# Optimization experiments

Measured on AMD Instinct MI355X. Metric: run time of the kernel, lower is better.

The kernel has to match this reference:

```python
import jax, jax.numpy as jnp
import numpy as np
from jax import lax

DN = ('NCHW', 'OIHW', 'NCHW')

def conv3x3(x, w):
    return lax.conv_general_dilated(x, w, (1, 1), 'SAME', dimension_numbers=DN)

def conv1x1(x, w, b):
    # w: [O, C], x: [B, C, H, W]
    return jnp.einsum('oc,bchw->bohw', w, x) + b[None, :, None, None]

def bn_relu(x, p):
    # p: [2, C] -> (scale, shift), eval-mode folded BatchNorm + ReLU
    return jax.nn.relu(x * p[0][None, :, None, None] + p[1][None, :, None, None])

def pam(y, Wb, bb, Wc, bc, Wd, bd, alpha):
    B, C, H, W = y.shape
    n = H * W
    b_ = conv1x1(y, Wb, bb).reshape(B, -1, n)   # [B, C/8, N]
    c_ = conv1x1(y, Wc, bc).reshape(B, -1, n)   # [B, C/8, N]
    d_ = conv1x1(y, Wd, bd).reshape(B, C, n)    # [B, C, N]
    energy = jnp.einsum('bkn,bkm->bnm', b_, c_)  # [B, N, N]
    attn = jax.nn.softmax(energy, axis=-1)
    feat = jnp.einsum('bcm,bnm->bcn', d_, attn).reshape(B, C, H, W)
    return alpha[0] * feat + y

def cam(y, beta):
    B, C, H, W = y.shape
    xf = y.reshape(B, C, H * W)
    energy = jnp.einsum('bcn,bdn->bcd', xf, xf)  # [B, C, C]
    energy = jnp.max(energy, axis=-1, keepdims=True) - energy
    attn = jax.nn.softmax(energy, axis=-1)
    feat = jnp.einsum('bcd,bdn->bcn', attn, xf).reshape(B, C, H, W)
    return beta[0] * feat + y

def reference(x, Wp1, bnp1, Wc1, bnc1, Wb, bb, Wc, bc, Wd, bd, alpha, beta,
              Wp2, bnp2, Wc2, bnc2, Wout, bout, Wp3, bp3, Wc3, bc3):
    feat_p = bn_relu(conv3x3(x, Wp1), bnp1)
    feat_p = pam(feat_p, Wb, bb, Wc, bc, Wd, bd, alpha)
    feat_p = bn_relu(conv3x3(feat_p, Wp2), bnp2)

    feat_c = bn_relu(conv3x3(x, Wc1), bnc1)
    feat_c = cam(feat_c, beta)
    feat_c = bn_relu(conv3x3(feat_c, Wc2), bnc2)

    fusion = feat_p + feat_c
    out_main = jax.nn.sigmoid(conv1x1(fusion, Wout, bout))
    out_p = jax.nn.sigmoid(conv1x1(feat_p, Wp3, bp3))
    out_c = jax.nn.sigmoid(conv1x1(feat_c, Wc3, bc3))
    return (out_main, out_p, out_c)

def setup_inputs() -> dict:
    key = jax.random.key(0)
    ks = jax.random.split(key, 24)
    Cin, Ci, Ck, NC = 512, 128, 16, 19
    B, H, W = 8, 64, 64
    s = lambda k, shape, scale=0.05: jax.random.normal(k, shape, jnp.float32) * scale
    return {
        'x': jax.random.normal(ks[0], (B, Cin, H, W), jnp.float32),
        'Wp1': s(ks[1], (Ci, Cin, 3, 3)), 'bnp1': jnp.stack([jnp.ones(Ci), jnp.zeros(Ci)]),
        'Wc1': s(ks[2], (Ci, Cin, 3, 3)), 'bnc1': jnp.stack([jnp.ones(Ci), jnp.zeros(Ci)]),
        'Wb': s(ks[3], (Ck, Ci)), 'bb': s(ks[4], (Ck,)),
        'Wc': s(ks[5], (Ck, Ci)), 'bc': s(ks[6], (Ck,)),
        'Wd': s(ks[7], (Ci, Ci)), 'bd': s(ks[8], (Ci,)),
        'alpha': jax.random.normal(ks[9], (1,), jnp.float32) * 0.5,
        'beta': jax.random.normal(ks[10], (1,), jnp.float32) * 0.5,
        'Wp2': s(ks[11], (Ci, Ci, 3, 3)), 'bnp2': jnp.stack([jnp.ones(Ci), jnp.zeros(Ci)]),
        'Wc2': s(ks[12], (Ci, Ci, 3, 3)), 'bnc2': jnp.stack([jnp.ones(Ci), jnp.zeros(Ci)]),
        'Wout': s(ks[13], (NC, Ci)), 'bout': s(ks[14], (NC,)),
        'Wp3': s(ks[15], (NC, Ci)), 'bp3': s(ks[16], (NC,)),
        'Wc3': s(ks[17], (NC, Ci)), 'bc3': s(ks[18], (NC,)),
    }
```

## Files before the change

kernel.cpp:

```cpp
#include <hip/hip_runtime.h>
#include <math.h>


typedef __attribute__((ext_vector_type(8)))  short short8;
typedef __attribute__((ext_vector_type(16))) float f32x16;

__device__ inline unsigned short f2bf(float f) {
    union { float f; unsigned u; } v; v.f = f;
    unsigned r = v.u + 0x7fffu + ((v.u >> 16) & 1u);
    return (unsigned short)(r >> 16);
}
__device__ inline float bf2f(unsigned short h) {
    union { unsigned u; float f; } v; v.u = ((unsigned)h) << 16;
    return v.f;
}

__global__ __launch_bounds__(256) void wpack_kernel(
    const float* __restrict__ W, unsigned short* __restrict__ wp, int Cin, int total)
{
    int idx = blockIdx.x * 256 + threadIdx.x;
    if (idx >= total) return;
    int chunk = idx / 18432;
    int rem   = idx - chunk * 18432;
    int tap   = rem >> 11;
    int rem2  = rem & 2047;
    int co    = rem2 >> 4;
    int ci    = rem2 & 15;
    int cin   = (chunk << 4) + ci;
    wp[idx] = f2bf(W[((size_t)co * Cin + cin) * 9 + tap]);
}

__global__ __launch_bounds__(256) void wpack_split_kernel(
    const float* __restrict__ W, unsigned short* __restrict__ wph,
    unsigned short* __restrict__ wpl, int Cin, int total)
{
    int idx = blockIdx.x * 256 + threadIdx.x;
    if (idx >= total) return;
    int chunk = idx / 18432;
    int rem   = idx - chunk * 18432;
    int tap   = rem >> 11;
    int rem2  = rem & 2047;
    int co    = rem2 >> 4;
    int ci    = rem2 & 15;
    int cin   = (chunk << 4) + ci;
    float w = W[((size_t)co * Cin + cin) * 9 + tap];
    unsigned short hi = f2bf(w);
    wph[idx] = hi;
    wpl[idx] = f2bf(w - bf2f(hi));
}

__global__ __launch_bounds__(256) void conv3x3_mfma(
    const void* __restrict__ xin, int in_is_fp32, int Cin,
    const unsigned short* __restrict__ wpack, const float* __restrict__ bn,
    float* __restrict__ out_f32, unsigned short* __restrict__ out_bf)
{
    const int t   = threadIdx.x;
    const int w   = t >> 6;
    const int wy  = w >> 1;
    const int wx  = w & 1;
    const int ln  = t & 63;
    const int l31 = ln & 31;
    const int g   = ln >> 5;
    const int y0  = blockIdx.x << 1;
    const int co0 = blockIdx.y << 6;
    const int b   = blockIdx.z;

    __shared__ __align__(16) unsigned short Xl[4 * 66 * 16];
    __shared__ __align__(16) unsigned short Wl[9 * 64 * 16];

    const f32x16 zero = {0,0,0,0,0,0,0,0,0,0,0,0,0,0,0,0};
    f32x16 acc0 = zero, acc1 = zero;

    const int nchunks = Cin >> 4;
    for (int ch = 0; ch < nchunks; ++ch) {
        const int cin0 = ch << 4;
        for (int pid = t; pid < 264; pid += 256) {
            int r  = pid / 66;
            int xc = pid - r * 66;
            int gy = y0 - 1 + r;
            int gx = xc - 1;
            unsigned short tmp[16];
            if ((unsigned)gy < 64u && (unsigned)gx < 64u) {
                if (in_is_fp32) {
                    const float* src = (const float*)xin
                        + (((size_t)b * Cin + cin0) << 12) + (gy << 6) + gx;
#pragma unroll
                    for (int c = 0; c < 16; c++) tmp[c] = f2bf(src[(size_t)c << 12]);
                } else {
                    const unsigned short* src = (const unsigned short*)xin
                        + (((size_t)b * Cin + cin0) << 12) + (gy << 6) + gx;
#pragma unroll
                    for (int c = 0; c < 16; c++) tmp[c] = src[(size_t)c << 12];
                }
            } else {
#pragma unroll
                for (int c = 0; c < 16; c++) tmp[c] = 0;
            }
            *(uint4*)&Xl[pid * 16 + 0] = ((uint4*)tmp)[0];
            *(uint4*)&Xl[pid * 16 + 8] = ((uint4*)tmp)[1];
        }
        {
            const uint4* wsrc = (const uint4*)wpack;
            const int base = ch * 2304 + (co0 << 1);
            for (int idx = t; idx < 1152; idx += 256)
                ((uint4*)Wl)[idx] = wsrc[base + ((idx >> 7) << 8) + (idx & 127)];
        }
        __syncthreads();

#pragma unroll 3
        for (int tap = 0; tap < 9; ++tap) {
            const int dy = tap / 3, dx = tap - dy * 3;
            short8 a = *(const short8*)&Wl[((tap << 6) + (wy << 5) + l31) * 16 + (g << 3)];
            const int row = wx + dy;
            short8 b0 = *(const short8*)&Xl[(row * 66 + l31 + dx) * 16 + (g << 3)];
            short8 b1 = *(const short8*)&Xl[(row * 66 + l31 + 32 + dx) * 16 + (g << 3)];
            acc0 = __builtin_amdgcn_mfma_f32_32x32x16_bf16(a, b0, acc0, 0, 0, 0);
            acc1 = __builtin_amdgcn_mfma_f32_32x32x16_bf16(a, b1, acc1, 0, 0, 0);
        }
        __syncthreads();
    }

    const int y = y0 + wx;
#pragma unroll
    for (int j = 0; j < 2; j++) {
        const f32x16 a = j ? acc1 : acc0;
#pragma unroll
        for (int r = 0; r < 16; r++) {
            int co = co0 + (wy << 5) + (r & 3) + ((r >> 2) << 3) + (g << 2);
            int x  = (j << 5) + l31;
            float v = fmaf(a[r], bn[co], bn[128 + co]);
            v = v > 0.f ? v : 0.f;
            size_t o = (((size_t)b * 128 + co) << 12) + (y << 6) + x;
            if (out_f32) out_f32[o] = v;
            if (out_bf)  out_bf[o]  = f2bf(v);
        }
    }
}

__global__ __launch_bounds__(256) void conv3x3_mfma_hilo(
    const float* __restrict__ xin, int Cin,
    const unsigned short* __restrict__ wph, const unsigned short* __restrict__ wpl,
    const float* __restrict__ bn, float* __restrict__ out_f32,
    unsigned short* __restrict__ outh, unsigned short* __restrict__ outl)
{
    const int t   = threadIdx.x;
    const int w   = t >> 6;
    const int wy  = w >> 1;
    const int wx  = w & 1;
    const int ln  = t & 63;
    const int l31 = ln & 31;
    const int g   = ln >> 5;
    const int y0  = blockIdx.x << 1;
    const int co0 = blockIdx.y << 6;
    const int b   = blockIdx.z;

    __shared__ __align__(16) unsigned short Xh[4 * 66 * 16];
    __shared__ __align__(16) unsigned short Xo[4 * 66 * 16];
    __shared__ __align__(16) unsigned short Wh[9 * 64 * 16];
    __shared__ __align__(16) unsigned short Wo[9 * 64 * 16];

    const f32x16 zero = {0,0,0,0,0,0,0,0,0,0,0,0,0,0,0,0};
    f32x16 acc0 = zero, acc1 = zero;

    const int nchunks = Cin >> 4;
    for (int ch = 0; ch < nchunks; ++ch) {
        const int cin0 = ch << 4;
        for (int pid = t; pid < 264; pid += 256) {
            int r  = pid / 66;
            int xc = pid - r * 66;
            int gy = y0 - 1 + r;
            int gx = xc - 1;
            unsigned short th[16], tl[16];
            if ((unsigned)gy < 64u && (unsigned)gx < 64u) {
                const float* src = xin + (((size_t)b * Cin + cin0) << 12) + (gy << 6) + gx;
#pragma unroll
                for (int c = 0; c < 16; c++) {
                    float f = src[(size_t)c << 12];
                    unsigned short hi = f2bf(f);
                    th[c] = hi;
                    tl[c] = f2bf(f - bf2f(hi));
                }
            } else {
#pragma unroll
                for (int c = 0; c < 16; c++) { th[c] = 0; tl[c] = 0; }
            }
            *(uint4*)&Xh[pid * 16 + 0] = ((uint4*)th)[0];
            *(uint4*)&Xh[pid * 16 + 8] = ((uint4*)th)[1];
            *(uint4*)&Xo[pid * 16 + 0] = ((uint4*)tl)[0];
            *(uint4*)&Xo[pid * 16 + 8] = ((uint4*)tl)[1];
        }
        {
            const uint4* sh = (const uint4*)wph;
            const uint4* sl = (const uint4*)wpl;
            const int base = ch * 2304 + (co0 << 1);
            for (int idx = t; idx < 1152; idx += 256) {
                int o = base + ((idx >> 7) << 8) + (idx & 127);
                ((uint4*)Wh)[idx] = sh[o];
                ((uint4*)Wo)[idx] = sl[o];
            }
        }
        __syncthreads();

#pragma unroll 1
        for (int tap = 0; tap < 9; ++tap) {
            const int dy = tap / 3, dx = tap - dy * 3;
            const int wi = ((tap << 6) + (wy << 5) + l31) * 16 + (g << 3);
            const int row = wx + dy;
            const int xi0 = (row * 66 + l31 + dx) * 16 + (g << 3);
            const int xi1 = (row * 66 + l31 + 32 + dx) * 16 + (g << 3);
            short8 ah = *(const short8*)&Wh[wi];
            short8 al = *(const short8*)&Wo[wi];
            short8 b0h = *(const short8*)&Xh[xi0];
            short8 b1h = *(const short8*)&Xh[xi1];
            short8 b0l = *(const short8*)&Xo[xi0];
            short8 b1l = *(const short8*)&Xo[xi1];
            acc0 = __builtin_amdgcn_mfma_f32_32x32x16_bf16(ah, b0h, acc0, 0, 0, 0);
            acc1 = __builtin_amdgcn_mfma_f32_32x32x16_bf16(ah, b1h, acc1, 0, 0, 0);
            acc0 = __builtin_amdgcn_mfma_f32_32x32x16_bf16(ah, b0l, acc0, 0, 0, 0);
            acc1 = __builtin_amdgcn_mfma_f32_32x32x16_bf16(ah, b1l, acc1, 0, 0, 0);
            acc0 = __builtin_amdgcn_mfma_f32_32x32x16_bf16(al, b0h, acc0, 0, 0, 0);
            acc1 = __builtin_amdgcn_mfma_f32_32x32x16_bf16(al, b1h, acc1, 0, 0, 0);
        }
        __syncthreads();
    }

    const int y = y0 + wx;
#pragma unroll
    for (int j = 0; j < 2; j++) {
        const f32x16 a = j ? acc1 : acc0;
#pragma unroll
        for (int r = 0; r < 16; r++) {
            int co = co0 + (wy << 5) + (r & 3) + ((r >> 2) << 3) + (g << 2);
            int x  = (j << 5) + l31;
            float v = fmaf(a[r], bn[co], bn[128 + co]);
            v = v > 0.f ? v : 0.f;
            size_t o = (((size_t)b * 128 + co) << 12) + (y << 6) + x;
            out_f32[o] = v;
            if (outh) {
                unsigned short hi = f2bf(v);
                outh[o] = hi;
                outl[o] = f2bf(v - bf2f(hi));
            }
        }
    }
}

__global__ __launch_bounds__(256) void cam_energy_mfma(
    const unsigned short* __restrict__ bh, const unsigned short* __restrict__ bl,
    float* __restrict__ egy_part)
{
    const int t   = threadIdx.x;
    const int w   = t >> 6;
    const int ln  = t & 63;
    const int l31 = ln & 31;
    const int g   = ln >> 5;
    const int i0  = (blockIdx.x >> 2) << 5;
    const int j0  = (blockIdx.x & 3) << 5;
    const int nseg = blockIdx.y;
    const int b   = blockIdx.z;

    __shared__ float red[4][64][17];

    const f32x16 zero = {0,0,0,0,0,0,0,0,0,0,0,0,0,0,0,0};
    f32x16 acc = zero;
    const int nb = (nseg << 9) + (w << 7) + (g << 3);
    const size_t ri = ((size_t)b * 128 + i0 + l31) << 12;
    const size_t rj = ((size_t)b * 128 + j0 + l31) << 12;

#pragma unroll
    for (int c = 0; c < 8; c++) {
        const int n0 = nb + (c << 4);
        short8 ah  = *(const short8*)(bh + ri + n0);
        short8 al  = *(const short8*)(bl + ri + n0);
        short8 bhf = *(const short8*)(bh + rj + n0);
        short8 blf = *(const short8*)(bl + rj + n0);
        acc = __builtin_amdgcn_mfma_f32_32x32x16_bf16(ah, bhf, acc, 0, 0, 0);
        acc = __builtin_amdgcn_mfma_f32_32x32x16_bf16(ah, blf, acc, 0, 0, 0);
        acc = __builtin_amdgcn_mfma_f32_32x32x16_bf16(al, bhf, acc, 0, 0, 0);
    }
#pragma unroll
    for (int r = 0; r < 16; r++) red[w][ln][r] = acc[r];
    __syncthreads();

    const int lane = t & 63;
    const int rq   = t >> 6;
    float* base = egy_part + (((size_t)(nseg * 8 + b)) << 14);
#pragma unroll
    for (int e = 0; e < 4; e++) {
        const int reg = (rq << 2) + e;
        float v = red[0][lane][reg] + red[1][lane][reg]
                + red[2][lane][reg] + red[3][lane][reg];
        const int i = i0 + (reg & 3) + ((reg >> 2) << 3) + ((lane >> 5) << 2);
        base[i * 128 + j0 + (lane & 31)] = v;
    }
}

__global__ __launch_bounds__(256) void cam_softmax_fused(
    const float* __restrict__ egy_part, float* __restrict__ egy)
{
    const int b   = blockIdx.x;
    const int rg  = blockIdx.y;
    const int t   = threadIdx.x;
    const int row = (rg << 4) + (t >> 4);
    const int jg  = t & 15;

    float e[8];
#pragma unroll
    for (int jj = 0; jj < 8; jj++) e[jj] = 0.f;
    for (int seg = 0; seg < 8; seg++) {
        const float* p = egy_part + (((size_t)(seg * 8 + b)) << 14) + row * 128 + (jg << 3);
#pragma unroll
        for (int jj = 0; jj < 8; jj++) e[jj] += p[jj];
    }
    float mn = e[0];
#pragma unroll
    for (int jj = 1; jj < 8; jj++) mn = fminf(mn, e[jj]);
#pragma unroll
    for (int k = 1; k < 16; k <<= 1) mn = fminf(mn, __shfl_xor(mn, k));
    float s = 0.f;
#pragma unroll
    for (int jj = 0; jj < 8; jj++) { float p = __expf(mn - e[jj]); e[jj] = p; s += p; }
#pragma unroll
    for (int k = 1; k < 16; k <<= 1) s += __shfl_xor(s, k);
    const float inv = 1.f / s;
    float* orow = egy + ((size_t)b << 14) + row * 128 + (jg << 3);
#pragma unroll
    for (int jj = 0; jj < 8; jj++) orow[jj] = e[jj] * inv;
}

__global__ __launch_bounds__(256) void pam_qk_1x1(
    const float* __restrict__ A, const float* __restrict__ Wb, const float* __restrict__ bb,
    const float* __restrict__ Wc, const float* __restrict__ bc,
    unsigned short* __restrict__ qt, unsigned short* __restrict__ kt)
{
    __shared__ float wl[2 * 16 * 128];
    __shared__ float bl[32];
    const int t = threadIdx.x;
    const int n = (blockIdx.x << 8) + t;
    const int b = blockIdx.y;
    for (int idx = t; idx < 2048; idx += 256) { wl[idx] = Wb[idx]; wl[2048 + idx] = Wc[idx]; }
    if (t < 16) { bl[t] = bb[t]; bl[16 + t] = bc[t]; }
    __syncthreads();
    float ab[16], ac[16];
#pragma unroll
    for (int k = 0; k < 16; k++) { ab[k] = 0.f; ac[k] = 0.f; }
    for (int chn = 0; chn < 128; ++chn) {
        float a = A[(((size_t)b * 128 + chn) << 12) + n];
#pragma unroll
        for (int k = 0; k < 16; k++) {
            ab[k] = fmaf(wl[k * 128 + chn], a, ab[k]);
            ac[k] = fmaf(wl[2048 + k * 128 + chn], a, ac[k]);
        }
    }
    unsigned short uq[16], uk[16];
#pragma unroll
    for (int k = 0; k < 16; k++) {
        uq[k] = f2bf(ab[k] + bl[k]);
        uk[k] = f2bf(ac[k] + bl[16 + k]);
    }
    size_t row = (size_t)b * 4096 + n;
    ((uint4*)qt)[row * 2 + 0] = ((uint4*)uq)[0];
    ((uint4*)qt)[row * 2 + 1] = ((uint4*)uq)[1];
    ((uint4*)kt)[row * 2 + 0] = ((uint4*)uk)[0];
    ((uint4*)kt)[row * 2 + 1] = ((uint4*)uk)[1];
}

__global__ __launch_bounds__(256) void pam_v_1x1(
    const float* __restrict__ A, const float* __restrict__ Wd, const float* __restrict__ bd,
    unsigned short* __restrict__ vb)
{
    __shared__ float wl[32 * 128];
    __shared__ float bl[32];
    const int t   = threadIdx.x;
    const int n   = (blockIdx.x << 8) + t;
    const int co0 = blockIdx.y << 5;
    const int b   = blockIdx.z;
    for (int idx = t; idx < 4096; idx += 256) {
        int c2 = idx >> 7, chv = idx & 127;
        wl[idx] = Wd[(co0 + c2) * 128 + chv];
    }
    if (t < 32) bl[t] = bd[co0 + t];
    __syncthreads();
    float acc[32];
#pragma unroll
    for (int k = 0; k < 32; k++) acc[k] = 0.f;
    for (int chn = 0; chn < 128; ++chn) {
        float a = A[(((size_t)b * 128 + chn) << 12) + n];
#pragma unroll
        for (int k = 0; k < 32; k++) acc[k] = fmaf(wl[k * 128 + chn], a, acc[k]);
    }
#pragma unroll
    for (int k = 0; k < 32; k++)
        vb[(((size_t)b * 128 + co0 + k) << 12) + n] = f2bf(acc[k] + bl[k]);
}

__global__ __launch_bounds__(256) void pam_rowmax(
    const unsigned short* __restrict__ qt, const unsigned short* __restrict__ kt,
    float* __restrict__ rowmax)
{
    const int t  = threadIdx.x;
    const int w  = t >> 6;
    const int L  = t & 63;
    const int ln = L & 31;
    const int g  = L >> 5;
    const int b  = blockIdx.y;
    const int n0 = blockIdx.x << 5;
    __shared__ float red[4][32];

    const f32x16 zero = {0,0,0,0,0,0,0,0,0,0,0,0,0,0,0,0};
    short8 qfrag = *(const short8*)(qt + (((size_t)b * 4096 + n0 + ln) << 4) + (g << 3));

    float mx = -INFINITY;
    for (int mq = (w << 5); mq < 4096; mq += 128) {
        short8 kfrag = *(const short8*)(kt + (((size_t)b * 4096 + mq + ln) << 4) + (g << 3));
        f32x16 s = __builtin_amdgcn_mfma_f32_32x32x16_bf16(kfrag, qfrag, zero, 0, 0, 0);
#pragma unroll
        for (int r = 0; r < 16; r++) mx = fmaxf(mx, s[r]);
    }
    mx = fmaxf(mx, __shfl_xor(mx, 32));
    if (L < 32) red[w][L] = mx;
    __syncthreads();
    if (t < 32) {
        float m = fmaxf(fmaxf(red[0][t], red[1][t]), fmaxf(red[2][t], red[3][t]));
        rowmax[((size_t)b << 12) + n0 + t] = m;
    }
}

__global__ __launch_bounds__(256) void pam_attn_mfma(
    const unsigned short* __restrict__ qt, const unsigned short* __restrict__ kt,
    const unsigned short* __restrict__ vb, const float* __restrict__ rowmax,
    const float* __restrict__ alpha, const float* __restrict__ Y,
    unsigned short* __restrict__ outb)
{
    const int t  = threadIdx.x;
    const int w  = t >> 6;
    const int L  = t & 63;
    const int ln = L & 31;
    const int g  = L >> 5;
    const int b  = blockIdx.y;
    const int n0 = blockIdx.x << 5;
    const int c0 = w << 5;

    __shared__ unsigned short Pf[16 * 256];
    __shared__ float red[4][32];

    const f32x16 zero = {0,0,0,0,0,0,0,0,0,0,0,0,0,0,0,0};
    short8 qfrag = *(const short8*)(qt + (((size_t)b * 4096 + n0 + ln) << 4) + (g << 3));
    const float rm = rowmax[((size_t)b << 12) + n0 + ln];
    const float al = alpha[0];

    f32x16 acc = zero;
    float rs = 0.f;

    for (int m0 = 0; m0 < 4096; m0 += 128) {
        const int mq = m0 + (w << 5);
        short8 kfrag = *(const short8*)(kt + (((size_t)b * 4096 + mq + ln) << 4) + (g << 3));
        f32x16 s = __builtin_amdgcn_mfma_f32_32x32x16_bf16(kfrag, qfrag, zero, 0, 0, 0);

        float p[16];
#pragma unroll
        for (int r = 0; r < 16; r++) { p[r] = __expf(s[r] - rm); rs += p[r]; }
        float xx[16];
#pragma unroll
        for (int r = 0; r < 16; r++) xx[r] = __shfl_xor(p[r], 32);

        unsigned short f0[8], f1[8];
#pragma unroll
        for (int i = 0; i < 4; i++) {
            f0[i]     = f2bf(g ? xx[4 + i]  : p[i]);
            f0[4 + i] = f2bf(g ? p[4 + i]   : xx[i]);
            f1[i]     = f2bf(g ? xx[12 + i] : p[8 + i]);
            f1[4 + i] = f2bf(g ? p[12 + i]  : xx[8 + i]);
        }
        *(short8*)(&Pf[((w << 2) + g) * 256 + (ln << 3)])     = *(short8*)f0;
        *(short8*)(&Pf[((w << 2) + 2 + g) * 256 + (ln << 3)]) = *(short8*)f1;
        __syncthreads();

#pragma unroll
        for (int kk = 0; kk < 8; kk++) {
            short8 pfrag = *(const short8*)(&Pf[((kk << 1) + g) * 256 + (ln << 3)]);
            short8 vfrag = *(const short8*)(vb + (((size_t)b * 128 + c0 + ln) << 12)
                                               + m0 + (kk << 4) + (g << 3));
            acc = __builtin_amdgcn_mfma_f32_32x32x16_bf16(vfrag, pfrag, acc, 0, 0, 0);
        }
        __syncthreads();
    }

    rs += __shfl_xor(rs, 32);
    if (L < 32) red[w][L] = rs;
    __syncthreads();
    const float inv = 1.f / (red[0][ln] + red[1][ln] + red[2][ln] + red[3][ln]);
    const int n = n0 + ln;
#pragma unroll
    for (int r = 0; r < 16; r++) {
        int c = c0 + (r & 3) + ((r >> 2) << 3) + (g << 2);
        size_t idx = (((size_t)b * 128 + c) << 12) + n;
        outb[idx] = f2bf(fmaf(al, acc[r] * inv, Y[idx]));
    }
}

__global__ __launch_bounds__(256) void cam_feat(
    const float* __restrict__ attn, const float* __restrict__ Bf,
    const float* __restrict__ beta, float* __restrict__ outf)
{
    const int t  = threadIdx.x;
    const int n  = (blockIdx.x << 8) + t;
    const int c0 = blockIdx.y << 5;
    const int b  = blockIdx.z;
    __shared__ float al[32 * 128];
    for (int idx = t; idx < 4096; idx += 256)
        al[idx] = attn[(size_t)b * 16384 + (c0 + (idx >> 7)) * 128 + (idx & 127)];
    __syncthreads();
    float acc[32];
#pragma unroll
    for (int k = 0; k < 32; k++) acc[k] = 0.f;
    for (int d = 0; d < 128; ++d) {
        float v = Bf[(((size_t)b * 128 + d) << 12) + n];
#pragma unroll
        for (int k = 0; k < 32; k++) acc[k] = fmaf(al[k * 128 + d], v, acc[k]);
    }
    float be = beta[0];
#pragma unroll
    for (int k = 0; k < 32; k++) {
        size_t idx = (((size_t)b * 128 + c0 + k) << 12) + n;
        outf[idx] = fmaf(be, acc[k], Bf[idx]);
    }
}

__global__ __launch_bounds__(256) void heads(
    const float* __restrict__ FP, const float* __restrict__ FC,
    const float* __restrict__ Wout, const float* __restrict__ bout,
    const float* __restrict__ Wp3, const float* __restrict__ bp3,
    const float* __restrict__ Wc3, const float* __restrict__ bc3,
    float* __restrict__ out)
{
    const int t = threadIdx.x;
    const int n = (blockIdx.x << 8) + t;
    const int b = blockIdx.y;
    __shared__ float wl[3 * 19 * 128];
    __shared__ float bl[3 * 19];
    for (int idx = t; idx < 2432; idx += 256) {
        wl[idx]        = Wout[idx];
        wl[2432 + idx] = Wp3[idx];
        wl[4864 + idx] = Wc3[idx];
    }
    if (t < 19) { bl[t] = bout[t]; bl[19 + t] = bp3[t]; bl[38 + t] = bc3[t]; }
    __syncthreads();
    float am[19], ap[19], ac[19];
#pragma unroll
    for (int o = 0; o < 19; o++) { am[o] = 0.f; ap[o] = 0.f; ac[o] = 0.f; }
    for (int chn = 0; chn < 128; ++chn) {
        float pv = FP[(((size_t)b * 128 + chn) << 12) + n];
        float cv = FC[(((size_t)b * 128 + chn) << 12) + n];
        float fv = pv + cv;
#pragma unroll
        for (int o = 0; o < 19; o++) {
            am[o] = fmaf(wl[o * 128 + chn], fv, am[o]);
            ap[o] = fmaf(wl[2432 + o * 128 + chn], pv, ap[o]);
            ac[o] = fmaf(wl[4864 + o * 128 + chn], cv, ac[o]);
        }
    }
    const size_t OS = (size_t)8 * 19 * 4096;
#pragma unroll
    for (int o = 0; o < 19; o++) {
        size_t base = (((size_t)b * 19 + o) << 12) + n;
        out[base]          = 1.f / (1.f + __expf(-(am[o] + bl[o])));
        out[OS + base]     = 1.f / (1.f + __expf(-(ap[o] + bl[19 + o])));
        out[2 * OS + base] = 1.f / (1.f + __expf(-(ac[o] + bl[38 + o])));
    }
}

extern "C" void kernel_launch(void* const* d_in, const int* in_sizes, int n_in,
                              void* d_out, int out_size, void* d_ws, size_t ws_size,
                              hipStream_t stream)
{
    const float* x     = (const float*)d_in[0];
    const float* Wp1   = (const float*)d_in[1];
    const float* bnp1  = (const float*)d_in[2];
    const float* Wc1   = (const float*)d_in[3];
    const float* bnc1  = (const float*)d_in[4];
    const float* Wb    = (const float*)d_in[5];
    const float* bb    = (const float*)d_in[6];
    const float* Wc    = (const float*)d_in[7];
    const float* bcv   = (const float*)d_in[8];
    const float* Wd    = (const float*)d_in[9];
    const float* bd    = (const float*)d_in[10];
    const float* alpha = (const float*)d_in[11];
    const float* beta  = (const float*)d_in[12];
    const float* Wp2   = (const float*)d_in[13];
    const float* bnp2  = (const float*)d_in[14];
    const float* Wc2   = (const float*)d_in[15];
    const float* bnc2  = (const float*)d_in[16];
    const float* Wout  = (const float*)d_in[17];
    const float* bo    = (const float*)d_in[18];
    const float* Wp3   = (const float*)d_in[19];
    const float* bp3   = (const float*)d_in[20];
    const float* Wc3   = (const float*)d_in[21];
    const float* bc3   = (const float*)d_in[22];
    float* out = (float*)d_out;

    char* ws = (char*)d_ws;
    const size_t MB = 1u << 20;
    const size_t W1SZ = (size_t)32 * 18432 * 2;
    const size_t W2SZ = (size_t)8 * 18432 * 2;
    float*          bufA     = (float*)(ws);
    float*          bufB     = (float*)(ws + 16 * MB);
    unsigned short* vb       = (unsigned short*)(ws + 32 * MB);
    float*          egy_part = (float*)(ws + 40 * MB);
    float*          bufD     = (float*)(ws + 32 * MB);
    unsigned short* bh       = (unsigned short*)(ws + 48 * MB);
    unsigned short* blo      = (unsigned short*)(ws + 56 * MB);
    unsigned short* pam_bf   = (unsigned short*)(ws + 48 * MB);
    float*          camf     = (float*)(ws + 48 * MB);
    unsigned short* qt       = (unsigned short*)(ws + 64 * MB);
    unsigned short* kt       = (unsigned short*)(ws + 65 * MB);
    float*          rowmax   = (float*)(ws + 66 * MB);
    float*          egy      = (float*)(ws + 66 * MB + (1u << 17));
    unsigned short* wp1      = (unsigned short*)(ws + 67 * MB);
    unsigned short* wc1h     = (unsigned short*)(ws + 67 * MB + W1SZ);
    unsigned short* wc1l     = (unsigned short*)(ws + 67 * MB + 2 * W1SZ);
    unsigned short* wp2      = (unsigned short*)(ws + 67 * MB + 3 * W1SZ);
    unsigned short* wc2h     = (unsigned short*)(ws + 67 * MB + 3 * W1SZ + W2SZ);
    unsigned short* wc2l     = (unsigned short*)(ws + 67 * MB + 3 * W1SZ + 2 * W2SZ);

    dim3 blk(256);
    const int n1 = 32 * 18432;
    const int n2 = 8 * 18432;
    wpack_kernel<<<dim3((n1 + 255) / 256), blk, 0, stream>>>(Wp1, wp1, 512, n1);
    wpack_kernel<<<dim3((n2 + 255) / 256), blk, 0, stream>>>(Wp2, wp2, 128, n2);
    wpack_split_kernel<<<dim3((n1 + 255) / 256), blk, 0, stream>>>(Wc1, wc1h, wc1l, 512, n1);
    wpack_split_kernel<<<dim3((n2 + 255) / 256), blk, 0, stream>>>(Wc2, wc2h, wc2l, 128, n2);

    conv3x3_mfma<<<dim3(32, 2, 8), blk, 0, stream>>>(x, 1, 512, wp1, bnp1, bufA, (unsigned short*)0);
    conv3x3_mfma_hilo<<<dim3(32, 2, 8), blk, 0, stream>>>(x, 512, wc1h, wc1l, bnc1, bufB, bh, blo);
    cam_energy_mfma<<<dim3(16, 8, 8), blk, 0, stream>>>(bh, blo, egy_part);
    cam_softmax_fused<<<dim3(8, 8), blk, 0, stream>>>(egy_part, egy);
    pam_qk_1x1<<<dim3(16, 8), blk, 0, stream>>>(bufA, Wb, bb, Wc, bcv, qt, kt);
    pam_v_1x1<<<dim3(16, 4, 8), blk, 0, stream>>>(bufA, Wd, bd, vb);
    pam_rowmax<<<dim3(128, 8), blk, 0, stream>>>(qt, kt, rowmax);
    pam_attn_mfma<<<dim3(128, 8), blk, 0, stream>>>(qt, kt, vb, rowmax, alpha, bufA, pam_bf);
    conv3x3_mfma<<<dim3(32, 2, 8), blk, 0, stream>>>(pam_bf, 0, 128, wp2, bnp2, bufD, (unsigned short*)0);
    cam_feat<<<dim3(16, 4, 8), blk, 0, stream>>>(egy, bufB, beta, camf);
    conv3x3_mfma_hilo<<<dim3(32, 2, 8), blk, 0, stream>>>(camf, 128, wc2h, wc2l, bnc2, bufA,
                                                          (unsigned short*)0, (unsigned short*)0);
    heads<<<dim3(16, 8), blk, 0, stream>>>(bufD, bufA, Wout, bo, Wp3, bp3, Wc3, bc3, out);
}
```

Before: 842.6 us.

## Merge both first-stage 3x3 convs into one kernel sharing input tiles

Adds a merged conv kernel that computes the PAM branch (bf16) and CAM branch (hi/lo split bf16) convolutions over x from one shared input tile, so the 512-channel fp32 input is read and converted only once. The weight packing and the LDS layout are reorganised into separate halves per 8-channel group. Weight tiles are now moved with direct global-to-LDS loads instead of going through registers. The merged kernel uses more LDS and four accumulators, which may lower occupancy.

```diff
diff --git a/kernel.cpp b/kernel.cpp
--- a/kernel.cpp
+++ b/kernel.cpp
@@ -4,6 +4,10 @@
 
 typedef __attribute__((ext_vector_type(8)))  short short8;
 typedef __attribute__((ext_vector_type(16))) float f32x16;
+
+#define GLD_LDS16(gp, lp) __builtin_amdgcn_global_load_lds( \
+    (const __attribute__((address_space(1))) void*)(gp),    \
+    (__attribute__((address_space(3))) void*)(lp), 16, 0, 0)
 
 __device__ inline unsigned short f2bf(float f) {
     union { float f; unsigned u; } v; v.f = f;
@@ -24,9 +28,10 @@
     int rem   = idx - chunk * 18432;
     int tap   = rem >> 11;
     int rem2  = rem & 2047;
-    int co    = rem2 >> 4;
-    int ci    = rem2 & 15;
-    int cin   = (chunk << 4) + ci;
+    int g     = rem2 >> 10;
+    int co    = (rem2 >> 3) & 127;
+    int ci8   = rem2 & 7;
+    int cin   = (chunk << 4) + (g << 3) + ci8;
     wp[idx] = f2bf(W[((size_t)co * Cin + cin) * 9 + tap]);
 }
 
@@ -40,9 +45,10 @@
     int rem   = idx - chunk * 18432;
     int tap   = rem >> 11;
     int rem2  = rem & 2047;
-    int co    = rem2 >> 4;
-    int ci    = rem2 & 15;
-    int cin   = (chunk << 4) + ci;
+    int g     = rem2 >> 10;
+    int co    = (rem2 >> 3) & 127;
+    int ci8   = rem2 & 7;
+    int cin   = (chunk << 4) + (g << 3) + ci8;
     float w = W[((size_t)co * Cin + cin) * 9 + tap];
     unsigned short hi = f2bf(w);
     wph[idx] = hi;
@@ -65,8 +71,8 @@
     const int co0 = blockIdx.y << 6;
     const int b   = blockIdx.z;
 
-    __shared__ __align__(16) unsigned short Xl[4 * 66 * 16];
-    __shared__ __align__(16) unsigned short Wl[9 * 64 * 16];
+    __shared__ __align__(16) unsigned short Xl[2 * 264 * 8];
+    __shared__ __align__(16) unsigned short Wl[9 * 1024];
 
     const f32x16 zero = {0,0,0,0,0,0,0,0,0,0,0,0,0,0,0,0};
     f32x16 acc0 = zero, acc1 = zero;
@@ -96,24 +102,29 @@
 #pragma unroll
                 for (int c = 0; c < 16; c++) tmp[c] = 0;
             }
-            *(uint4*)&Xl[pid * 16 + 0] = ((uint4*)tmp)[0];
-            *(uint4*)&Xl[pid * 16 + 8] = ((uint4*)tmp)[1];
+            *(uint4*)&Xl[(pid << 3)]        = ((uint4*)tmp)[0];
+            *(uint4*)&Xl[2112 + (pid << 3)] = ((uint4*)tmp)[1];
         }
         {
             const uint4* wsrc = (const uint4*)wpack;
-            const int base = ch * 2304 + (co0 << 1);
-            for (int idx = t; idx < 1152; idx += 256)
-                ((uint4*)Wl)[idx] = wsrc[base + ((idx >> 7) << 8) + (idx & 127)];
+            const int base = ch * 2304 + co0;
+            for (int u0 = (w << 6); u0 < 1152; u0 += 256) {
+                const int u = u0 + ln;
+                GLD_LDS16(wsrc + base + ((u >> 7) << 8) + (((u >> 6) & 1) << 7) + (u & 63),
+                          ((uint4*)Wl) + u0);
+            }
         }
         __syncthreads();
 
 #pragma unroll 3
         for (int tap = 0; tap < 9; ++tap) {
             const int dy = tap / 3, dx = tap - dy * 3;
-            short8 a = *(const short8*)&Wl[((tap << 6) + (wy << 5) + l31) * 16 + (g << 3)];
+            const int wi = (tap << 10) + (g << 9) + (((wy << 5) + l31) << 3);
             const int row = wx + dy;
-            short8 b0 = *(const short8*)&Xl[(row * 66 + l31 + dx) * 16 + (g << 3)];
-            short8 b1 = *(const short8*)&Xl[(row * 66 + l31 + 32 + dx) * 16 + (g << 3)];
+            const int xb = ((row * 66 + l31 + dx) << 3) + (g ? 2112 : 0);
+            short8 a  = *(const short8*)&Wl[wi];
+            short8 b0 = *(const short8*)&Xl[xb];
+            short8 b1 = *(const short8*)&Xl[xb + 256];
             acc0 = __builtin_amdgcn_mfma_f32_32x32x16_bf16(a, b0, acc0, 0, 0, 0);
             acc1 = __builtin_amdgcn_mfma_f32_32x32x16_bf16(a, b1, acc1, 0, 0, 0);
         }
@@ -154,10 +165,10 @@
     const int co0 = blockIdx.y << 6;
     const int b   = blockIdx.z;
 
-    __shared__ __align__(16) unsigned short Xh[4 * 66 * 16];
-    __shared__ __align__(16) unsigned short Xo[4 * 66 * 16];
-    __shared__ __align__(16) unsigned short Wh[9 * 64 * 16];
-    __shared__ __align__(16) unsigned short Wo[9 * 64 * 16];
+    __shared__ __align__(16) unsigned short Xh[2 * 264 * 8];
+    __shared__ __align__(16) unsigned short Xo[2 * 264 * 8];
+    __shared__ __align__(16) unsigned short Wh[9 * 1024];
+    __shared__ __align__(16) unsigned short Wo[9 * 1024];
 
     const f32x16 zero = {0,0,0,0,0,0,0,0,0,0,0,0,0,0,0,0};
     f32x16 acc0 = zero, acc1 = zero;
@@ -184,19 +195,20 @@
 #pragma unroll
                 for (int c = 0; c < 16; c++) { th[c] = 0; tl[c] = 0; }
             }
-            *(uint4*)&Xh[pid * 16 + 0] = ((uint4*)th)[0];
-            *(uint4*)&Xh[pid * 16 + 8] = ((uint4*)th)[1];
-            *(uint4*)&Xo[pid * 16 + 0] = ((uint4*)tl)[0];
-            *(uint4*)&Xo[pid * 16 + 8] = ((uint4*)tl)[1];
+            *(uint4*)&Xh[(pid << 3)]        = ((uint4*)th)[0];
+            *(uint4*)&Xh[2112 + (pid << 3)] = ((uint4*)th)[1];
+            *(uint4*)&Xo[(pid << 3)]        = ((uint4*)tl)[0];
+            *(uint4*)&Xo[2112 + (pid << 3)] = ((uint4*)tl)[1];
         }
         {
             const uint4* sh = (const uint4*)wph;
             const uint4* sl = (const uint4*)wpl;
-            const int base = ch * 2304 + (co0 << 1);
-            for (int idx = t; idx < 1152; idx += 256) {
-                int o = base + ((idx >> 7) << 8) + (idx & 127);
-                ((uint4*)Wh)[idx] = sh[o];
-                ((uint4*)Wo)[idx] = sl[o];
+            const int base = ch * 2304 + co0;
+            for (int u0 = (w << 6); u0 < 1152; u0 += 256) {
+                const int u = u0 + ln;
+                const int o = base + ((u >> 7) << 8) + (((u >> 6) & 1) << 7) + (u & 63);
+                GLD_LDS16(sh + o, ((uint4*)Wh) + u0);
+                GLD_LDS16(sl + o, ((uint4*)Wo) + u0);
             }
         }
         __syncthreads();
@@ -204,16 +216,15 @@
 #pragma unroll 1
         for (int tap = 0; tap < 9; ++tap) {
             const int dy = tap / 3, dx = tap - dy * 3;
-            const int wi = ((tap << 6) + (wy << 5) + l31) * 16 + (g << 3);
+            const int wi = (tap << 10) + (g << 9) + (((wy << 5) + l31) << 3);
             const int row = wx + dy;
-            const int xi0 = (row * 66 + l31 + dx) * 16 + (g << 3);
-            const int xi1 = (row * 66 + l31 + 32 + dx) * 16 + (g << 3);
-            short8 ah = *(const short8*)&Wh[wi];
-            short8 al = *(const short8*)&Wo[wi];
-            short8 b0h = *(const short8*)&Xh[xi0];
-            short8 b1h = *(const short8*)&Xh[xi1];
-            short8 b0l = *(const short8*)&Xo[xi0];
-            short8 b1l = *(const short8*)&Xo[xi1];
+            const int xb = ((row * 66 + l31 + dx) << 3) + (g ? 2112 : 0);
+            short8 ah  = *(const short8*)&Wh[wi];
+            short8 al  = *(const short8*)&Wo[wi];
+            short8 b0h = *(const short8*)&Xh[xb];
+            short8 b1h = *(const short8*)&Xh[xb + 256];
+            short8 b0l = *(const short8*)&Xo[xb];
+            short8 b1l = *(const short8*)&Xo[xb + 256];
             acc0 = __builtin_amdgcn_mfma_f32_32x32x16_bf16(ah, b0h, acc0, 0, 0, 0);
             acc1 = __builtin_amdgcn_mfma_f32_32x32x16_bf16(ah, b1h, acc1, 0, 0, 0);
             acc0 = __builtin_amdgcn_mfma_f32_32x32x16_bf16(ah, b0l, acc0, 0, 0, 0);
@@ -241,6 +252,123 @@
                 outh[o] = hi;
                 outl[o] = f2bf(v - bf2f(hi));
             }
+        }
+    }
+}
+
+__global__ __launch_bounds__(256) void conv3x3_merged(
+    const float* __restrict__ xin,
+    const unsigned short* __restrict__ wpp,
+    const unsigned short* __restrict__ wph, const unsigned short* __restrict__ wpl,
+    const float* __restrict__ bnp, const float* __restrict__ bnc,
+    float* __restrict__ outP, float* __restrict__ outC,
+    unsigned short* __restrict__ outh, unsigned short* __restrict__ outl)
+{
+    const int t   = threadIdx.x;
+    const int w   = t >> 6;
+    const int wy  = w >> 1;
+    const int wx  = w & 1;
+    const int ln  = t & 63;
+    const int l31 = ln & 31;
+    const int g   = ln >> 5;
+    const int y0  = blockIdx.x << 1;
+    const int co0 = blockIdx.y << 6;
+    const int b   = blockIdx.z;
+
+    __shared__ __align__(16) unsigned short Xh[2 * 264 * 8];
+    __shared__ __align__(16) unsigned short Xo[2 * 264 * 8];
+    __shared__ __align__(16) unsigned short Wp[9 * 1024];
+    __shared__ __align__(16) unsigned short Wh[9 * 1024];
+    __shared__ __align__(16) unsigned short Wo[9 * 1024];
+
+    const f32x16 zero = {0,0,0,0,0,0,0,0,0,0,0,0,0,0,0,0};
+    f32x16 ap0 = zero, ap1 = zero, ac0 = zero, ac1 = zero;
+
+    for (int ch = 0; ch < 32; ++ch) {
+        const int cin0 = ch << 4;
+        for (int pid = t; pid < 264; pid += 256) {
+            int r  = pid / 66;
+            int xc = pid - r * 66;
+            int gy = y0 - 1 + r;
+            int gx = xc - 1;
+            unsigned short th[16], tl[16];
+            if ((unsigned)gy < 64u && (unsigned)gx < 64u) {
+                const float* src = xin + (((size_t)b * 512 + cin0) << 12) + (gy << 6) + gx;
+#pragma unroll
+                for (int c = 0; c < 16; c++) {
+                    float f = src[(size_t)c << 12];
+                    unsigned short hi = f2bf(f);
+                    th[c] = hi;
+                    tl[c] = f2bf(f - bf2f(hi));
+                }
+            } else {
+#pragma unroll
+                for (int c = 0; c < 16; c++) { th[c] = 0; tl[c] = 0; }
+            }
+            *(uint4*)&Xh[(pid << 3)]        = ((uint4*)th)[0];
+            *(uint4*)&Xh[2112 + (pid << 3)] = ((uint4*)th)[1];
+            *(uint4*)&Xo[(pid << 3)]        = ((uint4*)tl)[0];
+            *(uint4*)&Xo[2112 + (pid << 3)] = ((uint4*)tl)[1];
+        }
+        {
+            const uint4* sp = (const uint4*)wpp;
+            const uint4* sh = (const uint4*)wph;
+            const uint4* sl = (const uint4*)wpl;
+            const int base = ch * 2304 + co0;
+            for (int u0 = (w << 6); u0 < 1152; u0 += 256) {
+                const int u = u0 + ln;
+                const int o = base + ((u >> 7) << 8) + (((u >> 6) & 1) << 7) + (u & 63);
+                GLD_LDS16(sp + o, ((uint4*)Wp) + u0);
+                GLD_LDS16(sh + o, ((uint4*)Wh) + u0);
+                GLD_LDS16(sl + o, ((uint4*)Wo) + u0);
+            }
+        }
+        __syncthreads();
+
+#pragma unroll 1
+        for (int tap = 0; tap < 9; ++tap) {
+            const int dy = tap / 3, dx = tap - dy * 3;
+            const int wi = (tap << 10) + (g << 9) + (((wy << 5) + l31) << 3);
+            const int row = wx + dy;
+            const int xb = ((row * 66 + l31 + dx) << 3) + (g ? 2112 : 0);
+            short8 vap = *(const short8*)&Wp[wi];
+            short8 vah = *(const short8*)&Wh[wi];
+            short8 val = *(const short8*)&Wo[wi];
+            short8 b0h = *(const short8*)&Xh[xb];
+            short8 b1h = *(const short8*)&Xh[xb + 256];
+            short8 b0l = *(const short8*)&Xo[xb];
+            short8 b1l = *(const short8*)&Xo[xb + 256];
+            ap0 = __builtin_amdgcn_mfma_f32_32x32x16_bf16(vap, b0h, ap0, 0, 0, 0);
+            ap1 = __builtin_amdgcn_mfma_f32_32x32x16_bf16(vap, b1h, ap1, 0, 0, 0);
+            ac0 = __builtin_amdgcn_mfma_f32_32x32x16_bf16(vah, b0h, ac0, 0, 0, 0);
+            ac1 = __builtin_amdgcn_mfma_f32_32x32x16_bf16(vah, b1h, ac1, 0, 0, 0);
+            ac0 = __builtin_amdgcn_mfma_f32_32x32x16_bf16(vah, b0l, ac0, 0, 0, 0);
+            ac1 = __builtin_amdgcn_mfma_f32_32x32x16_bf16(vah, b1l, ac1, 0, 0, 0);
+            ac0 = __builtin_amdgcn_mfma_f32_32x32x16_bf16(val, b0h, ac0, 0, 0, 0);
+            ac1 = __builtin_amdgcn_mfma_f32_32x32x16_bf16(val, b1h, ac1, 0, 0, 0);
+        }
+        __syncthreads();
+    }
+
+    const int y = y0 + wx;
+#pragma unroll
+    for (int j = 0; j < 2; j++) {
+        const f32x16 aP = j ? ap1 : ap0;
+        const f32x16 aC = j ? ac1 : ac0;
+#pragma unroll
+        for (int r = 0; r < 16; r++) {
+            int co = co0 + (wy << 5) + (r & 3) + ((r >> 2) << 3) + (g << 2);
+            int x  = (j << 5) + l31;
+            size_t o = (((size_t)b * 128 + co) << 12) + (y << 6) + x;
+            float vp = fmaf(aP[r], bnp[co], bnp[128 + co]);
+            vp = vp > 0.f ? vp : 0.f;
+            outP[o] = vp;
+            float vc = fmaf(aC[r], bnc[co], bnc[128 + co]);
+            vc = vc > 0.f ? vc : 0.f;
+            outC[o] = vc;
+            unsigned short hi = f2bf(vc);
+            outh[o] = hi;
+            outl[o] = f2bf(vc - bf2f(hi));
         }
     }
 }
@@ -631,8 +759,8 @@
     wpack_split_kernel<<<dim3((n1 + 255) / 256), blk, 0, stream>>>(Wc1, wc1h, wc1l, 512, n1);
     wpack_split_kernel<<<dim3((n2 + 255) / 256), blk, 0, stream>>>(Wc2, wc2h, wc2l, 128, n2);
 
-    conv3x3_mfma<<<dim3(32, 2, 8), blk, 0, stream>>>(x, 1, 512, wp1, bnp1, bufA, (unsigned short*)0);
-    conv3x3_mfma_hilo<<<dim3(32, 2, 8), blk, 0, stream>>>(x, 512, wc1h, wc1l, bnc1, bufB, bh, blo);
+    conv3x3_merged<<<dim3(32, 2, 8), blk, 0, stream>>>(x, wp1, wc1h, wc1l, bnp1, bnc1,
+                                                       bufA, bufB, bh, blo);
     cam_energy_mfma<<<dim3(16, 8, 8), blk, 0, stream>>>(bh, blo, egy_part);
     cam_softmax_fused<<<dim3(8, 8), blk, 0, stream>>>(egy_part, egy);
     pam_qk_1x1<<<dim3(16, 8), blk, 0, stream>>>(bufA, Wb, bb, Wc, bcv, qt, kt);
```

After: 816.2 us. 3.1% less time.
